# Performance work log

Measured on AMD Instinct MI355X. Metric: run time of the kernel, lower is better.

The kernel has to match this reference:

```python
import jax, jax.numpy as jnp
import numpy as np

D_IN = 2048
H1 = D_IN // 4      # 512
H2 = D_IN // 16     # 128
N_EXP = 8
N_CLS = 10
BATCH = 16384


def setup_inputs() -> dict:
    key = jax.random.key(0)
    ks = jax.random.split(key, 16)
    s = lambda k, shape, fan_in: jax.random.normal(k, shape, jnp.float32) / np.sqrt(fan_in)
    return {
        "fs": jax.random.normal(ks[0], (BATCH, D_IN // 2), jnp.float32),
        "fp": jax.random.normal(ks[1], (BATCH, D_IN // 2), jnp.float32),
        # gate MLP params (output = num_source, softmax)
        "gW1": s(ks[2], (D_IN, H1), D_IN), "gb1": jnp.zeros((H1,), jnp.float32),
        "gW2": s(ks[3], (H1, H2), H1),     "gb2": jnp.zeros((H2,), jnp.float32),
        "gW3": s(ks[4], (H2, N_EXP), H2), "gb3": jnp.zeros((N_EXP,), jnp.float32),
        # stacked expert MLP params (output = num classes, log_softmax)
        "eW1": s(ks[5], (N_EXP, D_IN, H1), D_IN), "eb1": jnp.zeros((N_EXP, H1), jnp.float32),
        "eW2": s(ks[6], (N_EXP, H1, H2), H1),     "eb2": jnp.zeros((N_EXP, H2), jnp.float32),
        "eW3": s(ks[7], (N_EXP, H2, N_CLS), H2),  "eb3": jnp.zeros((N_EXP, N_CLS), jnp.float32),
    }


def reference(fs, fp, gW1, gb1, gW2, gb2, gW3, gb3, eW1, eb1, eW2, eb2, eW3, eb3):
    features = jnp.concatenate([fs, fp], axis=-1)            # [B, D_IN]

    # Gate MLP on detached features (detach is a no-op for fwd), softmax output
    g = jax.nn.relu(features @ gW1 + gb1)
    g = jax.nn.relu(g @ gW2 + gb2)
    gate_outs = jax.nn.softmax(g @ gW3 + gb3, axis=-1)       # [B, E]

    # All experts as batched GEMMs over stacked weights, log_softmax output
    h = jax.nn.relu(jnp.einsum('bd,edh->beh', features, eW1) + eb1[None])   # [B, E, H1]
    h = jax.nn.relu(jnp.einsum('beh,ehk->bek', h, eW2) + eb2[None])         # [B, E, H2]
    logits = jnp.einsum('bek,eko->beo', h, eW3) + eb3[None]                 # [B, E, C]
    expert_outs = jax.nn.log_softmax(logits, axis=-1)                       # [B, E, C]

    # Gate-weighted sum over experts
    output = jnp.einsum('be,bec->bc', gate_outs, expert_outs)               # [B, C]
    return output, gate_outs
```

## Files before the change

kernel.cpp:

```cpp
#include <hip/hip_runtime.h>
#include <hip/hip_bf16.h>

#define B_SZ   16384
#define DIN    2048
#define H1_SZ  512
#define H2_SZ  128
#define N_EXP  8
#define N_CLS  10
#define N1     4608
#define N2     1152

typedef __attribute__((ext_vector_type(8))) __bf16 bf16x8;
typedef __attribute__((ext_vector_type(4))) float  floatx4;
typedef __attribute__((ext_vector_type(4))) short  short4v;
typedef __attribute__((ext_vector_type(8))) short  short8v;

__device__ __forceinline__ float bf2f(short s) {
  unsigned int u = ((unsigned int)(unsigned short)s) << 16;
  float f; __builtin_memcpy(&f, &u, 4); return f;
}

__global__ void convert_features_kernel(const float* __restrict__ fs,
                                        const float* __restrict__ fp,
                                        __hip_bfloat16* __restrict__ X) {
  const int nf4 = B_SZ * (DIN / 4);
  const float4* fs4 = (const float4*)fs;
  const float4* fp4 = (const float4*)fp;
  for (int i = blockIdx.x * blockDim.x + threadIdx.x; i < nf4;
       i += gridDim.x * blockDim.x) {
    int c = i & 511;
    int row = i >> 9;
    float4 v = (c < 256) ? fs4[(size_t)row * 256 + c]
                         : fp4[(size_t)row * 256 + (c - 256)];
    union { short4v v4; __hip_bfloat16 h[4]; } u;
    u.h[0] = __float2bfloat16(v.x);
    u.h[1] = __float2bfloat16(v.y);
    u.h[2] = __float2bfloat16(v.z);
    u.h[3] = __float2bfloat16(v.w);
    *(short4v*)(X + (size_t)i * 4) = u.v4;
  }
}

__global__ void transpose_convert_kernel(const float* __restrict__ expert_src,
                                         const float* __restrict__ gate_src,
                                         int K, int H, int E,
                                         __hip_bfloat16* __restrict__ out) {
  __shared__ float t[32][33];
  int k0 = blockIdx.x * 32;
  int n0 = blockIdx.y * 32;
  int e = n0 / H;
  const float* src; int h0;
  if (e < E) { src = expert_src + (size_t)e * K * H; h0 = n0 - e * H; }
  else       { src = gate_src;                       h0 = n0 - E * H; }
  int tx = threadIdx.x, ty = threadIdx.y;
  #pragma unroll
  for (int j = 0; j < 4; ++j) {
    int r = ty + j * 8;
    t[r][tx] = src[(size_t)(k0 + r) * H + h0 + tx];
  }
  __syncthreads();
  #pragma unroll
  for (int j = 0; j < 4; ++j) {
    int r = ty + j * 8;
    out[(size_t)(n0 + r) * K + k0 + tx] = __float2bfloat16(t[tx][r]);
  }
}

__device__ __forceinline__ void gemm_core(
    const __hip_bfloat16* __restrict__ A,  int lda,
    const __hip_bfloat16* __restrict__ BT, int K,
    const float* __restrict__ bias,
    __hip_bfloat16* __restrict__ O, int ldo) {
  __shared__ __align__(16) __hip_bfloat16 As[128 * 64];
  __shared__ __align__(16) __hip_bfloat16 Bs[128 * 64];

  const int tid  = threadIdx.x;
  const int lane = tid & 63;
  const int wave = tid >> 6;
  const int wm   = (wave >> 1) * 64;
  const int wn   = (wave & 1) * 64;
  const int lrow  = lane & 15;
  const int lquad = lane >> 4;

  floatx4 acc[4][4] = {};

  for (int k0 = 0; k0 < K; k0 += 64) {
    #pragma unroll
    for (int j = 0; j < 4; ++j) {
      int chunk = j * 256 + tid;
      int mi = chunk >> 3;
      int cs = chunk & 7;
      int cl = cs ^ (mi & 7);
      __builtin_amdgcn_global_load_lds(
          (const __attribute__((address_space(1))) unsigned int*)(A + (size_t)mi * lda + k0 + cl * 8),
          (__attribute__((address_space(3))) unsigned int*)(As + chunk * 8),
          16, 0, 0);
      __builtin_amdgcn_global_load_lds(
          (const __attribute__((address_space(1))) unsigned int*)(BT + (size_t)mi * K + k0 + cl * 8),
          (__attribute__((address_space(3))) unsigned int*)(Bs + chunk * 8),
          16, 0, 0);
    }
    __syncthreads();
    #pragma unroll
    for (int ks = 0; ks < 2; ++ks) {
      bf16x8 a[4], b[4];
      #pragma unroll
      for (int t = 0; t < 4; ++t) {
        int ar = wm + t * 16 + lrow;
        int br = wn + t * 16 + lrow;
        int ca = (ks * 4 + lquad) ^ (ar & 7);
        int cb = (ks * 4 + lquad) ^ (br & 7);
        a[t] = *(const bf16x8*)(As + ar * 64 + ca * 8);
        b[t] = *(const bf16x8*)(Bs + br * 64 + cb * 8);
      }
      #pragma unroll
      for (int mt = 0; mt < 4; ++mt)
        #pragma unroll
        for (int nt = 0; nt < 4; ++nt)
          acc[mt][nt] = __builtin_amdgcn_mfma_f32_16x16x32_bf16(
              a[mt], b[nt], acc[mt][nt], 0, 0, 0);
    }
    __syncthreads();
  }

  #pragma unroll
  for (int nt = 0; nt < 4; ++nt) {
    int col = wn + nt * 16 + lrow;
    float bv = bias[col];
    #pragma unroll
    for (int mt = 0; mt < 4; ++mt) {
      #pragma unroll
      for (int r = 0; r < 4; ++r) {
        int row = wm + mt * 16 + lquad * 4 + r;
        float v = acc[mt][nt][r] + bv;
        v = v > 0.f ? v : 0.f;
        O[(size_t)row * ldo + col] = __float2bfloat16(v);
      }
    }
  }
}

__global__ __launch_bounds__(256, 2) void gemm1_kernel(
    const __hip_bfloat16* __restrict__ X, const __hip_bfloat16* __restrict__ W1T,
    const float* __restrict__ eb1, const float* __restrict__ gb1,
    __hip_bfloat16* __restrict__ H1) {
  int m0 = blockIdx.y * 128;
  int n0 = blockIdx.x * 128;
  const float* bias = (n0 < N_EXP * H1_SZ) ? (eb1 + n0) : (gb1 + (n0 - N_EXP * H1_SZ));
  gemm_core(X + (size_t)m0 * DIN, DIN,
            W1T + (size_t)n0 * DIN, DIN,
            bias,
            H1 + (size_t)m0 * N1 + n0, N1);
}

__global__ __launch_bounds__(256, 2) void gemm2_kernel(
    const __hip_bfloat16* __restrict__ H1, const __hip_bfloat16* __restrict__ W2T,
    const float* __restrict__ eb2, const float* __restrict__ gb2,
    __hip_bfloat16* __restrict__ H2) {
  int m0 = blockIdx.y * 128;
  int z  = blockIdx.z;
  const float* bias = (z < N_EXP) ? (eb2 + z * H2_SZ) : gb2;
  gemm_core(H1 + (size_t)m0 * N1 + z * H1_SZ, N1,
            W2T + (size_t)z * H2_SZ * H1_SZ, H1_SZ,
            bias,
            H2 + (size_t)m0 * N2 + z * H2_SZ, N2);
}

__global__ __launch_bounds__(256) void layer3_kernel(
    const __hip_bfloat16* __restrict__ H2,
    const float* __restrict__ gW3, const float* __restrict__ gb3,
    const float* __restrict__ eW3, const float* __restrict__ eb3,
    float* __restrict__ out, float* __restrict__ gate_out) {
  int tid  = threadIdx.x;
  int j    = tid & 7;
  int rloc = tid >> 3;
  long row = (long)blockIdx.x * 32 + rloc;
  const __hip_bfloat16* hrow = H2 + row * N2;

  float accg = 0.f;
  float acc[N_CLS];
  #pragma unroll
  for (int c = 0; c < N_CLS; ++c) acc[c] = 0.f;

  #pragma unroll 4
  for (int k8 = 0; k8 < 16; ++k8) {
    short8v hg8 = *(const short8v*)(hrow + N_EXP * H2_SZ + k8 * 8);
    short8v he8 = *(const short8v*)(hrow + j * H2_SZ + k8 * 8);
    #pragma unroll
    for (int t = 0; t < 8; ++t) {
      int k = k8 * 8 + t;
      float hg = bf2f(hg8[t]);
      float he = bf2f(he8[t]);
      accg += hg * gW3[k * N_EXP + j];
      const float* w = eW3 + (size_t)(j * H2_SZ + k) * N_CLS;
      #pragma unroll
      for (int c = 0; c < N_CLS; ++c) acc[c] += he * w[c];
    }
  }

  float gj = accg + gb3[j];
  float mx = gj;
  mx = fmaxf(mx, __shfl_xor(mx, 1));
  mx = fmaxf(mx, __shfl_xor(mx, 2));
  mx = fmaxf(mx, __shfl_xor(mx, 4));
  float ex = __expf(gj - mx);
  float s = ex;
  s += __shfl_xor(s, 1);
  s += __shfl_xor(s, 2);
  s += __shfl_xor(s, 4);
  float gp = ex / s;

  float lg[N_CLS];
  float lm = -1e30f;
  #pragma unroll
  for (int c = 0; c < N_CLS; ++c) {
    lg[c] = acc[c] + eb3[j * N_CLS + c];
    lm = fmaxf(lm, lg[c]);
  }
  float es = 0.f;
  #pragma unroll
  for (int c = 0; c < N_CLS; ++c) es += __expf(lg[c] - lm);
  float lse = lm + __logf(es);

  float o[N_CLS];
  #pragma unroll
  for (int c = 0; c < N_CLS; ++c) o[c] = gp * (lg[c] - lse);
  #pragma unroll
  for (int c = 0; c < N_CLS; ++c) {
    o[c] += __shfl_xor(o[c], 1);
    o[c] += __shfl_xor(o[c], 2);
    o[c] += __shfl_xor(o[c], 4);
  }

  gate_out[row * N_EXP + j] = gp;
  if (j == 0) {
    #pragma unroll
    for (int c = 0; c < N_CLS; ++c) out[row * N_CLS + c] = o[c];
  }
}

extern "C" void kernel_launch(void* const* d_in, const int* in_sizes, int n_in,
                              void* d_out, int out_size, void* d_ws, size_t ws_size,
                              hipStream_t stream) {
  const float* fs  = (const float*)d_in[0];
  const float* fp  = (const float*)d_in[1];
  const float* gW1 = (const float*)d_in[2];
  const float* gb1 = (const float*)d_in[3];
  const float* gW2 = (const float*)d_in[4];
  const float* gb2 = (const float*)d_in[5];
  const float* gW3 = (const float*)d_in[6];
  const float* gb3 = (const float*)d_in[7];
  const float* eW1 = (const float*)d_in[8];
  const float* eb1 = (const float*)d_in[9];
  const float* eW2 = (const float*)d_in[10];
  const float* eb2 = (const float*)d_in[11];
  const float* eW3 = (const float*)d_in[12];
  const float* eb3 = (const float*)d_in[13];
  float* out = (float*)d_out;

  char* ws = (char*)d_ws;
  __hip_bfloat16* X   = (__hip_bfloat16*)ws;
  __hip_bfloat16* H2  = X;
  __hip_bfloat16* W1T = (__hip_bfloat16*)(ws + 67108864);
  __hip_bfloat16* W2T = (__hip_bfloat16*)(ws + 85983232);
  __hip_bfloat16* H1  = (__hip_bfloat16*)(ws + 87162880);

  convert_features_kernel<<<2048, 256, 0, stream>>>(fs, fp, X);
  transpose_convert_kernel<<<dim3(DIN / 32, N1 / 32), dim3(32, 8), 0, stream>>>(
      eW1, gW1, DIN, H1_SZ, N_EXP, W1T);
  transpose_convert_kernel<<<dim3(H1_SZ / 32, N2 / 32), dim3(32, 8), 0, stream>>>(
      eW2, gW2, H1_SZ, H2_SZ, N_EXP, W2T);
  gemm1_kernel<<<dim3(N1 / 128, B_SZ / 128), 256, 0, stream>>>(X, W1T, eb1, gb1, H1);
  gemm2_kernel<<<dim3(1, B_SZ / 128, N_EXP + 1), 256, 0, stream>>>(H1, W2T, eb2, gb2, H2);
  layer3_kernel<<<B_SZ / 32, 256, 0, stream>>>(H2, gW3, gb3, eW3, eb3,
                                               out, out + (size_t)B_SZ * N_CLS);
}
```

Measured before the change: 615.5 us.

## Rewrite layer-1 GEMM as 256x256 tile kernel with async LDS pipeline

```diff
diff --git a/kernel.cpp b/kernel.cpp
--- a/kernel.cpp
+++ b/kernel.cpp
@@ -66,6 +66,136 @@
   }
 }
 
+__device__ __forceinline__ void stage_sub(
+    const __hip_bfloat16* __restrict__ src, int ld, int row0, int kofs,
+    __hip_bfloat16* dst, int tid) {
+  #pragma unroll
+  for (int j = 0; j < 2; ++j) {
+    int c = j * 512 + tid;
+    int r = c >> 2;
+    int cl = (c & 3) ^ ((r >> 1) & 3);
+    __builtin_amdgcn_global_load_lds(
+        (const __attribute__((address_space(1))) unsigned int*)(
+            src + (size_t)(row0 + r) * ld + kofs + cl * 8),
+        (__attribute__((address_space(3))) unsigned int*)(dst + c * 8),
+        16, 0, 0);
+  }
+}
+
+__device__ __forceinline__ bf16x8 ldsfrag(const __hip_bfloat16* sub, int r, int lquad) {
+  int slot = lquad ^ ((r >> 1) & 3);
+  return *(const bf16x8*)(sub + r * 32 + slot * 8);
+}
+
+template <bool RDB, int MH>
+__device__ __forceinline__ void phase8(
+    const __hip_bfloat16* Asub, const __hip_bfloat16* Bsub,
+    floatx4 (&acc)[8][4], bf16x8 (&b)[4],
+    int wm, int wn, int lrow, int lquad,
+    const __hip_bfloat16* __restrict__ ssrc, int sld, int srow0, int skofs,
+    __hip_bfloat16* sdst, int tid) {
+  bf16x8 a[4];
+  #pragma unroll
+  for (int q = 0; q < 4; ++q)
+    a[q] = ldsfrag(Asub, wm + (MH * 4 + q) * 16 + lrow, lquad);
+  if (RDB) {
+    #pragma unroll
+    for (int nt = 0; nt < 4; ++nt)
+      b[nt] = ldsfrag(Bsub, wn + nt * 16 + lrow, lquad);
+  }
+  stage_sub(ssrc, sld, srow0, skofs, sdst, tid);
+  asm volatile("s_waitcnt vmcnt(8)" ::: "memory");
+  __builtin_amdgcn_s_barrier();
+  asm volatile("s_waitcnt lgkmcnt(0)" ::: "memory");
+  __builtin_amdgcn_sched_barrier(0);
+  __builtin_amdgcn_s_setprio(1);
+  #pragma unroll
+  for (int q = 0; q < 4; ++q)
+    #pragma unroll
+    for (int nt = 0; nt < 4; ++nt)
+      acc[MH * 4 + q][nt] = __builtin_amdgcn_mfma_f32_16x16x32_bf16(
+          a[q], b[nt], acc[MH * 4 + q][nt], 0, 0, 0);
+  __builtin_amdgcn_s_setprio(0);
+  __builtin_amdgcn_sched_barrier(0);
+  __builtin_amdgcn_s_barrier();
+  __builtin_amdgcn_sched_barrier(0);
+}
+
+__global__ __launch_bounds__(512, 2) void gemm1_kernel8(
+    const __hip_bfloat16* __restrict__ X, const __hip_bfloat16* __restrict__ W1T,
+    const float* __restrict__ eb1, const float* __restrict__ gb1,
+    __hip_bfloat16* __restrict__ H1) {
+  __shared__ __align__(16) __hip_bfloat16 lds[8][256 * 32];
+
+  const int tid  = threadIdx.x;
+  const int lane = tid & 63;
+  const int wave = tid >> 6;
+  const int wm   = (wave >> 2) * 128;
+  const int wn   = (wave & 3) * 64;
+  const int lrow  = lane & 15;
+  const int lquad = lane >> 4;
+
+  int flat = blockIdx.x;
+  int swz  = (flat & 7) * ((int)gridDim.x >> 3) + (flat >> 3);
+  int m0 = (swz / (N1 / 256)) * 256;
+  int n0 = (swz % (N1 / 256)) * 256;
+
+  floatx4 acc[8][4] = {};
+  bf16x8 b[4];
+
+  const int KT = DIN / 64;
+
+  stage_sub(X,   DIN, m0, 0,  lds[0], tid);
+  stage_sub(W1T, DIN, n0, 0,  lds[2], tid);
+  stage_sub(X,   DIN, m0, 32, lds[1], tid);
+  stage_sub(W1T, DIN, n0, 32, lds[3], tid);
+  stage_sub(X,   DIN, m0, 64, lds[4], tid);
+  stage_sub(W1T, DIN, n0, 64, lds[6], tid);
+  asm volatile("s_waitcnt vmcnt(8)" ::: "memory");
+  __builtin_amdgcn_s_barrier();
+  __builtin_amdgcn_sched_barrier(0);
+
+  for (int i = 0; i < KT / 2; ++i) {
+    int T  = 2 * i;
+    int k1 = (T + 1) * 64;
+    int k2 = min(T + 2, KT - 1) * 64;
+    int k3 = min(T + 3, KT - 1) * 64;
+    phase8<true,  0>(lds[0], lds[2], acc, b, wm, wn, lrow, lquad,
+                     X,   DIN, m0, k1 + 32, lds[5], tid);
+    phase8<false, 1>(lds[0], lds[2], acc, b, wm, wn, lrow, lquad,
+                     W1T, DIN, n0, k1 + 32, lds[7], tid);
+    phase8<true,  0>(lds[1], lds[3], acc, b, wm, wn, lrow, lquad,
+                     X,   DIN, m0, k2,      lds[0], tid);
+    phase8<false, 1>(lds[1], lds[3], acc, b, wm, wn, lrow, lquad,
+                     W1T, DIN, n0, k2,      lds[2], tid);
+    phase8<true,  0>(lds[4], lds[6], acc, b, wm, wn, lrow, lquad,
+                     X,   DIN, m0, k2 + 32, lds[1], tid);
+    phase8<false, 1>(lds[4], lds[6], acc, b, wm, wn, lrow, lquad,
+                     W1T, DIN, n0, k2 + 32, lds[3], tid);
+    phase8<true,  0>(lds[5], lds[7], acc, b, wm, wn, lrow, lquad,
+                     X,   DIN, m0, k3,      lds[4], tid);
+    phase8<false, 1>(lds[5], lds[7], acc, b, wm, wn, lrow, lquad,
+                     W1T, DIN, n0, k3,      lds[6], tid);
+  }
+
+  const float* bias = (n0 < N_EXP * H1_SZ) ? (eb1 + n0) : (gb1 + (n0 - N_EXP * H1_SZ));
+  #pragma unroll
+  for (int nt = 0; nt < 4; ++nt) {
+    int col = wn + nt * 16 + lrow;
+    float bv = bias[col];
+    #pragma unroll
+    for (int mt = 0; mt < 8; ++mt) {
+      #pragma unroll
+      for (int r = 0; r < 4; ++r) {
+        int row = m0 + wm + mt * 16 + lquad * 4 + r;
+        float v = acc[mt][nt][r] + bv;
+        v = v > 0.f ? v : 0.f;
+        H1[(size_t)row * N1 + n0 + col] = __float2bfloat16(v);
+      }
+    }
+  }
+}
+
 __device__ __forceinline__ void gemm_core(
     const __hip_bfloat16* __restrict__ A,  int lda,
     const __hip_bfloat16* __restrict__ BT, int K,
@@ -138,19 +268,6 @@
       }
     }
   }
-}
-
-__global__ __launch_bounds__(256, 2) void gemm1_kernel(
-    const __hip_bfloat16* __restrict__ X, const __hip_bfloat16* __restrict__ W1T,
-    const float* __restrict__ eb1, const float* __restrict__ gb1,
-    __hip_bfloat16* __restrict__ H1) {
-  int m0 = blockIdx.y * 128;
-  int n0 = blockIdx.x * 128;
-  const float* bias = (n0 < N_EXP * H1_SZ) ? (eb1 + n0) : (gb1 + (n0 - N_EXP * H1_SZ));
-  gemm_core(X + (size_t)m0 * DIN, DIN,
-            W1T + (size_t)n0 * DIN, DIN,
-            bias,
-            H1 + (size_t)m0 * N1 + n0, N1);
 }
 
 __global__ __launch_bounds__(256, 2) void gemm2_kernel(
@@ -270,7 +387,8 @@
       eW1, gW1, DIN, H1_SZ, N_EXP, W1T);
   transpose_convert_kernel<<<dim3(H1_SZ / 32, N2 / 32), dim3(32, 8), 0, stream>>>(
       eW2, gW2, H1_SZ, H2_SZ, N_EXP, W2T);
-  gemm1_kernel<<<dim3(N1 / 128, B_SZ / 128), 256, 0, stream>>>(X, W1T, eb1, gb1, H1);
+  gemm1_kernel8<<<dim3((N1 / 256) * (B_SZ / 256)), 512, 0, stream>>>(
+      X, W1T, eb1, gb1, H1);
   gemm2_kernel<<<dim3(1, B_SZ / 128, N_EXP + 1), 256, 0, stream>>>(H1, W2T, eb2, gb2, H2);
   layer3_kernel<<<B_SZ / 32, 256, 0, stream>>>(H2, gW3, gb3, eW3, eb3,
                                                out, out + (size_t)B_SZ * N_CLS);
```

Result: slower. 635.1 us (+3.2%).

## Swizzle gemm1 block order per XCD, nontemporal H1 stores, wider feature conversion

Applied to the files above, without the earlier changes.

```diff
diff --git a/kernel.cpp b/kernel.cpp
--- a/kernel.cpp
+++ b/kernel.cpp
@@ -23,21 +23,32 @@
 __global__ void convert_features_kernel(const float* __restrict__ fs,
                                         const float* __restrict__ fp,
                                         __hip_bfloat16* __restrict__ X) {
-  const int nf4 = B_SZ * (DIN / 4);
+  const int nf8 = B_SZ * (DIN / 8);
   const float4* fs4 = (const float4*)fs;
   const float4* fp4 = (const float4*)fp;
-  for (int i = blockIdx.x * blockDim.x + threadIdx.x; i < nf4;
+  for (int i = blockIdx.x * blockDim.x + threadIdx.x; i < nf8;
        i += gridDim.x * blockDim.x) {
-    int c = i & 511;
-    int row = i >> 9;
-    float4 v = (c < 256) ? fs4[(size_t)row * 256 + c]
-                         : fp4[(size_t)row * 256 + (c - 256)];
-    union { short4v v4; __hip_bfloat16 h[4]; } u;
-    u.h[0] = __float2bfloat16(v.x);
-    u.h[1] = __float2bfloat16(v.y);
-    u.h[2] = __float2bfloat16(v.z);
-    u.h[3] = __float2bfloat16(v.w);
-    *(short4v*)(X + (size_t)i * 4) = u.v4;
+    int c = i & 255;
+    int row = i >> 8;
+    float4 v0, v1;
+    if (c < 128) {
+      v0 = fs4[(size_t)row * 256 + 2 * c];
+      v1 = fs4[(size_t)row * 256 + 2 * c + 1];
+    } else {
+      int cc = c - 128;
+      v0 = fp4[(size_t)row * 256 + 2 * cc];
+      v1 = fp4[(size_t)row * 256 + 2 * cc + 1];
+    }
+    union { short8v v8; __hip_bfloat16 h[8]; } u;
+    u.h[0] = __float2bfloat16(v0.x);
+    u.h[1] = __float2bfloat16(v0.y);
+    u.h[2] = __float2bfloat16(v0.z);
+    u.h[3] = __float2bfloat16(v0.w);
+    u.h[4] = __float2bfloat16(v1.x);
+    u.h[5] = __float2bfloat16(v1.y);
+    u.h[6] = __float2bfloat16(v1.z);
+    u.h[7] = __float2bfloat16(v1.w);
+    *(short8v*)(X + (size_t)i * 8) = u.v8;
   }
 }
 
@@ -66,6 +77,7 @@
   }
 }
 
+template <bool NT>
 __device__ __forceinline__ void gemm_core(
     const __hip_bfloat16* __restrict__ A,  int lda,
     const __hip_bfloat16* __restrict__ BT, int K,
@@ -134,7 +146,14 @@
         int row = wm + mt * 16 + lquad * 4 + r;
         float v = acc[mt][nt][r] + bv;
         v = v > 0.f ? v : 0.f;
-        O[(size_t)row * ldo + col] = __float2bfloat16(v);
+        __hip_bfloat16 hv = __float2bfloat16(v);
+        if (NT) {
+          __builtin_nontemporal_store(
+              *reinterpret_cast<unsigned short*>(&hv),
+              reinterpret_cast<unsigned short*>(&O[(size_t)row * ldo + col]));
+        } else {
+          O[(size_t)row * ldo + col] = hv;
+        }
       }
     }
   }
@@ -144,13 +163,15 @@
     const __hip_bfloat16* __restrict__ X, const __hip_bfloat16* __restrict__ W1T,
     const float* __restrict__ eb1, const float* __restrict__ gb1,
     __hip_bfloat16* __restrict__ H1) {
-  int m0 = blockIdx.y * 128;
-  int n0 = blockIdx.x * 128;
+  int flat = blockIdx.x;
+  int swz  = (flat & 7) * 576 + (flat >> 3);
+  int m0 = (swz / 36) * 128;
+  int n0 = (swz % 36) * 128;
   const float* bias = (n0 < N_EXP * H1_SZ) ? (eb1 + n0) : (gb1 + (n0 - N_EXP * H1_SZ));
-  gemm_core(X + (size_t)m0 * DIN, DIN,
-            W1T + (size_t)n0 * DIN, DIN,
-            bias,
-            H1 + (size_t)m0 * N1 + n0, N1);
+  gemm_core<true>(X + (size_t)m0 * DIN, DIN,
+                  W1T + (size_t)n0 * DIN, DIN,
+                  bias,
+                  H1 + (size_t)m0 * N1 + n0, N1);
 }
 
 __global__ __launch_bounds__(256, 2) void gemm2_kernel(
@@ -160,10 +181,10 @@
   int m0 = blockIdx.y * 128;
   int z  = blockIdx.z;
   const float* bias = (z < N_EXP) ? (eb2 + z * H2_SZ) : gb2;
-  gemm_core(H1 + (size_t)m0 * N1 + z * H1_SZ, N1,
-            W2T + (size_t)z * H2_SZ * H1_SZ, H1_SZ,
-            bias,
-            H2 + (size_t)m0 * N2 + z * H2_SZ, N2);
+  gemm_core<false>(H1 + (size_t)m0 * N1 + z * H1_SZ, N1,
+                   W2T + (size_t)z * H2_SZ * H1_SZ, H1_SZ,
+                   bias,
+                   H2 + (size_t)m0 * N2 + z * H2_SZ, N2);
 }
 
 __global__ __launch_bounds__(256) void layer3_kernel(
@@ -270,7 +291,7 @@
       eW1, gW1, DIN, H1_SZ, N_EXP, W1T);
   transpose_convert_kernel<<<dim3(H1_SZ / 32, N2 / 32), dim3(32, 8), 0, stream>>>(
       eW2, gW2, H1_SZ, H2_SZ, N_EXP, W2T);
-  gemm1_kernel<<<dim3(N1 / 128, B_SZ / 128), 256, 0, stream>>>(X, W1T, eb1, gb1, H1);
+  gemm1_kernel<<<4608, 256, 0, stream>>>(X, W1T, eb1, gb1, H1);
   gemm2_kernel<<<dim3(1, B_SZ / 128, N_EXP + 1), 256, 0, stream>>>(H1, W2T, eb2, gb2, H2);
   layer3_kernel<<<B_SZ / 32, 256, 0, stream>>>(H2, gW3, gb3, eW3, eb3,
                                                out, out + (size_t)B_SZ * N_CLS);
```

Measured after the change: 707.1 us. 1.15x slower.
